# Optimization experiments

Measured on AMD Instinct MI355X. Metric: run time of the kernel, lower is better.

The kernel has to match this reference:

```python
import jax, jax.numpy as jnp
import numpy as np

NUM_MOL = 1024
KE = 14.399645351950548
KEHALF = KE / 2.0
CUTOFF = 10.0  # PhysNetCutOff(10.0)


def physnet_cutoff(d):
    # PhysNet smooth cutoff: 1 - 6u^5 + 15u^4 - 10u^3 for d < rc, else 0
    u = d / CUTOFF
    fc = 1.0 - 6.0 * u**5 + 15.0 * u**4 - 10.0 * u**3
    return jnp.where(d < CUTOFF, fc, 0.0)


def setup_inputs() -> dict:
    key = jax.random.key(0)
    k = jax.random.split(key, 5)
    N, E = 100000, 3200000
    # atomic numbers as floats in [1, 94]
    Z = jax.random.randint(k[0], (N,), 1, 95).astype(jnp.float32)
    # pair displacement vectors; norm ~ O(3) Angstrom, well inside cutoff
    r_ij = jax.random.normal(k[1], (E, 3), dtype=jnp.float32) * 2.0
    idx_i = jax.random.randint(k[2], (E,), 0, N, dtype=jnp.int32)
    idx_j = jax.random.randint(k[3], (E,), 0, N, dtype=jnp.int32)
    # per-atom molecule index, sorted (maxm = idx_m[-1] + 1 in the original)
    idx_m = jnp.sort(jax.random.randint(k[4], (N,), 0, NUM_MOL, dtype=jnp.int32))
    adiv = jnp.ones((1,), jnp.float32)
    apow = jnp.ones((1,), jnp.float32)
    a_vector = jnp.ones((4,), jnp.float32)
    c_vector = jnp.ones((4,), jnp.float32)
    return dict(Z=Z, r_ij=r_ij, idx_i=idx_i, idx_j=idx_j, idx_m=idx_m,
                adiv=adiv, apow=apow, a_vector=a_vector, c_vector=c_vector)


def reference(Z, r_ij, idx_i, idx_j, idx_m, adiv, apow, a_vector, c_vector):
    N = Z.shape[0]
    d = jnp.linalg.norm(r_ij, axis=1)                      # (E,)
    cut = physnet_cutoff(d)                                # (E,)
    z = Z ** jax.nn.softplus(apow[0])                      # (N,)
    a = (z[idx_i] + z[idx_j]) * jax.nn.softplus(adiv[0])   # (E,)
    a_comp = jax.nn.softplus(a_vector)[:, None] * a        # (4, E)
    c = jax.nn.softplus(c_vector)
    c_normed = c / jnp.sum(jnp.abs(c))                     # L1-normalize over dim 0
    f_temp = jnp.einsum('k,ke->e', c_normed, jnp.exp(-a_comp * d))  # (E,)
    f = f_temp * cut
    zizj = Z[idx_i] * Z[idx_j]
    e_edge = KEHALF * f * zizj / d                          # (E,)
    y_atom = jax.ops.segment_sum(e_edge, idx_i, num_segments=N)        # (N,)
    y = jax.ops.segment_sum(y_atom, idx_m, num_segments=NUM_MOL)       # (NUM_MOL,)
    return y
```

## Files before the change

### kernel.cpp

```cpp
#include <hip/hip_runtime.h>

#define NUM_MOL 1024
#define KEHALF 7.199822675975274f
#define RCUT 10.0f
#define ZS_CAP 130048

__device__ __forceinline__ float softplus_f(float x) {
    return (x > 20.0f) ? x : __logf(1.0f + __expf(x));
}

__device__ __forceinline__ float uni(float x) {
    return __int_as_float(__builtin_amdgcn_readfirstlane(__float_as_int(x)));
}


struct SmemT {
    float zptab[256];
    unsigned char zs[ZS_CAP];
};

__global__ __launch_bounds__(1024, 4) void zbl_edge_lds(
    const float4* __restrict__ r4,
    const int4* __restrict__ idx_i4,
    const int4* __restrict__ idx_j4,
    const int* __restrict__ idx_i,
    const int* __restrict__ idx_j,
    const float* __restrict__ r_ij,
    const float* __restrict__ Z,
    const int* __restrict__ idx_m,
    const float* __restrict__ adiv,
    const float* __restrict__ apow,
    const float* __restrict__ a_vector,
    const float* __restrict__ c_vector,
    float* __restrict__ y, int N, int E)
{
    __shared__ SmemT sm;
    const int tid = threadIdx.x;

    {
        const int nv4 = N >> 2;
        const float4* Z4 = (const float4*)Z;
        uchar4* dst = (uchar4*)sm.zs;
        for (int k = tid; k < nv4; k += blockDim.x) {
            const float4 zv = Z4[k];
            uchar4 pk;
            pk.x = (unsigned char)(int)zv.x;
            pk.y = (unsigned char)(int)zv.y;
            pk.z = (unsigned char)(int)zv.z;
            pk.w = (unsigned char)(int)zv.w;
            dst[k] = pk;
        }
        for (int k = (nv4 << 2) + tid; k < N; k += blockDim.x)
            sm.zs[k] = (unsigned char)(int)Z[k];
        if (tid < 256) {
            const float p = softplus_f(apow[0]);
            sm.zptab[tid] = (tid > 0) ? __powf((float)tid, p) : 0.0f;
        }
    }

    const float sp_adiv = uni(softplus_f(adiv[0]));
    const float sa0 = uni(softplus_f(a_vector[0]));
    const float sa1 = uni(softplus_f(a_vector[1]));
    const float sa2 = uni(softplus_f(a_vector[2]));
    const float sa3 = uni(softplus_f(a_vector[3]));
    float c0 = softplus_f(c_vector[0]);
    float c1 = softplus_f(c_vector[1]);
    float c2 = softplus_f(c_vector[2]);
    float c3 = softplus_f(c_vector[3]);
    const float cinv = 1.0f / (fabsf(c0) + fabsf(c1) + fabsf(c2) + fabsf(c3));
    const float k0 = uni(c0 * cinv);
    const float k1 = uni(c1 * cinv);
    const float k2 = uni(c2 * cinv);
    const float k3 = uni(c3 * cinv);
    const float samin = uni(fminf(fminf(sa0, sa1), fminf(sa2, sa3)));

    __syncthreads();

    auto edge1 = [&](int i, int j, float d2) {
        const int zi = sm.zs[i];
        const int zj = sm.zs[j];
        const float zpi = sm.zptab[zi];
        const float zpj = sm.zptab[zj];
        const float rinv = rsqrtf(d2);
        const float d = d2 * rinv;
        const float ad = (zpi + zpj) * sp_adiv * d;
        if (ad * samin < 104.0f) {
            const float u = d * (1.0f / RCUT);
            const float u3 = u * u * u;
            float fc = 1.0f + u3 * (-10.0f + u * (15.0f - 6.0f * u));
            fc = (d < RCUT) ? fc : 0.0f;
            const float ft = k0 * __expf(-sa0 * ad) + k1 * __expf(-sa1 * ad)
                           + k2 * __expf(-sa2 * ad) + k3 * __expf(-sa3 * ad);
            const float ee = KEHALF * ft * fc * (float)(zi * zj) * rinv;
            if (ee != 0.0f) atomicAdd(&y[idx_m[i]], ee);
        }
    };
    auto edge4 = [&](const int4& vi, const int4& vj,
                     const float4& r0, const float4& r1, const float4& r2) {
        edge1(vi.x, vj.x, r0.x * r0.x + r0.y * r0.y + r0.z * r0.z);
        edge1(vi.y, vj.y, r0.w * r0.w + r1.x * r1.x + r1.y * r1.y);
        edge1(vi.z, vj.z, r1.z * r1.z + r1.w * r1.w + r2.x * r2.x);
        edge1(vi.w, vj.w, r2.y * r2.y + r2.z * r2.z + r2.w * r2.w);
    };

    const int t = blockIdx.x * blockDim.x + tid;
    const int nthr = gridDim.x * blockDim.x;
    const int E4 = E >> 2;

#define LOADG(s, g) \
    int4 vi##s, vj##s; float4 ra##s, rb##s, rc##s; \
    const bool act##s = (g) < E4; \
    if (act##s) { vi##s = idx_i4[(g)]; vj##s = idx_j4[(g)]; \
        ra##s = r4[3 * (g) + 0]; rb##s = r4[3 * (g) + 1]; rc##s = r4[3 * (g) + 2]; }
#define COMPG(s) if (act##s) edge4(vi##s, vj##s, ra##s, rb##s, rc##s);

    for (int gb = t; gb < E4; gb += 4 * nthr) {
        const int g0 = gb;
        const int g1 = gb + nthr;
        const int g2 = gb + 2 * nthr;
        const int g3 = gb + 3 * nthr;
        LOADG(0, g0) LOADG(1, g1) LOADG(2, g2) LOADG(3, g3)
        COMPG(0) COMPG(1) COMPG(2) COMPG(3)
    }
#undef LOADG
#undef COMPG

    for (int e = (E4 << 2) + t; e < E; e += nthr) {
        const float x  = r_ij[3 * e + 0];
        const float yy = r_ij[3 * e + 1];
        const float zz = r_ij[3 * e + 2];
        edge1(idx_i[e], idx_j[e], x * x + yy * yy + zz * zz);
    }
}

__global__ __launch_bounds__(256) void zbl_edge_kernel_nows(
    const float* __restrict__ r_ij,
    const int* __restrict__ idx_i,
    const int* __restrict__ idx_j,
    const float* __restrict__ Z,
    const int* __restrict__ idx_m,
    const float* __restrict__ adiv,
    const float* __restrict__ apow,
    const float* __restrict__ a_vector,
    const float* __restrict__ c_vector,
    float* __restrict__ y, int E)
{
    __shared__ float bins[NUM_MOL];
    for (int b = threadIdx.x; b < NUM_MOL; b += blockDim.x) bins[b] = 0.0f;
    __syncthreads();

    const float sp_apow = softplus_f(apow[0]);
    const float sp_adiv = softplus_f(adiv[0]);
    const float sa0 = softplus_f(a_vector[0]);
    const float sa1 = softplus_f(a_vector[1]);
    const float sa2 = softplus_f(a_vector[2]);
    const float sa3 = softplus_f(a_vector[3]);
    float c0 = softplus_f(c_vector[0]);
    float c1 = softplus_f(c_vector[1]);
    float c2 = softplus_f(c_vector[2]);
    float c3 = softplus_f(c_vector[3]);
    const float cs = fabsf(c0) + fabsf(c1) + fabsf(c2) + fabsf(c3);
    const float cinv = 1.0f / cs;
    c0 *= cinv; c1 *= cinv; c2 *= cinv; c3 *= cinv;

    const int stride = gridDim.x * blockDim.x;
    for (int e = blockIdx.x * blockDim.x + threadIdx.x; e < E; e += stride) {
        const int i = idx_i[e];
        const int j = idx_j[e];
        const float zi = Z[i];
        const float zj = Z[j];
        const float x  = r_ij[3 * e + 0];
        const float yy = r_ij[3 * e + 1];
        const float zz = r_ij[3 * e + 2];
        const float d = sqrtf(x * x + yy * yy + zz * zz);

        const float u = d * (1.0f / RCUT);
        const float u3 = u * u * u;
        float fc = 1.0f + u3 * (-10.0f + u * (15.0f - 6.0f * u));
        fc = (d < RCUT) ? fc : 0.0f;

        const float a = (__powf(zi, sp_apow) + __powf(zj, sp_apow)) * sp_adiv;
        const float ad = a * d;
        const float ft = c0 * __expf(-sa0 * ad) + c1 * __expf(-sa1 * ad)
                       + c2 * __expf(-sa2 * ad) + c3 * __expf(-sa3 * ad);

        const float ee = KEHALF * ft * fc * zi * zj / d;
        if (ee != 0.0f) atomicAdd(&bins[idx_m[i]], ee);
    }

    __syncthreads();
    for (int b = threadIdx.x; b < NUM_MOL; b += blockDim.x) {
        const float v = bins[b];
        if (v != 0.0f) atomicAdd(&y[b], v);
    }
}

extern "C" void kernel_launch(void* const* d_in, const int* in_sizes, int n_in,
                              void* d_out, int out_size, void* d_ws, size_t ws_size,
                              hipStream_t stream) {
    const float* Z        = (const float*)d_in[0];
    const float* r_ij     = (const float*)d_in[1];
    const int*   idx_i    = (const int*)d_in[2];
    const int*   idx_j    = (const int*)d_in[3];
    const int*   idx_m    = (const int*)d_in[4];
    const float* adiv     = (const float*)d_in[5];
    const float* apow     = (const float*)d_in[6];
    const float* a_vector = (const float*)d_in[7];
    const float* c_vector = (const float*)d_in[8];
    float* y = (float*)d_out;

    const int N = in_sizes[0];
    const int E = in_sizes[1] / 3;

    hipMemsetAsync(y, 0, (size_t)out_size * sizeof(float), stream);

    if (N <= ZS_CAP) {
        zbl_edge_lds<<<256, 1024, 0, stream>>>(
            (const float4*)r_ij, (const int4*)idx_i, (const int4*)idx_j,
            idx_i, idx_j, r_ij, Z, idx_m, adiv, apow, a_vector, c_vector,
            y, N, E);
    } else {
        zbl_edge_kernel_nows<<<2048, 256, 0, stream>>>(r_ij, idx_i, idx_j, Z, idx_m,
                                                       adiv, apow, a_vector, c_vector, y, E);
    }
}
```

Before: 128.7 us.

## Move per-atom Z byte table from per-block LDS to a global L2-resident workspace

Adds a small prep kernel that packs Z into a uint8 array and builds a pow-table pre-scaled by softplus(adiv) in the workspace. The edge kernel then gathers Z bytes from global memory (L2) instead of having every one of the 256 blocks copy the whole 100K-entry array into about 130KB of LDS. This removes the large per-block staging cost and the LDS-driven single-block occupancy, and launches 2048 blocks of 256 threads. It also computes sqrt only and defers rsqrt until the exponential threshold passes, and drops the 4-way load batching. The trade-off is random global gathers through L2 in place of LDS reads, plus one extra kernel launch.

```diff
diff --git a/kernel.cpp b/kernel.cpp
--- a/kernel.cpp
+++ b/kernel.cpp
@@ -3,7 +3,6 @@
 #define NUM_MOL 1024
 #define KEHALF 7.199822675975274f
 #define RCUT 10.0f
-#define ZS_CAP 130048
 
 __device__ __forceinline__ float softplus_f(float x) {
     return (x > 20.0f) ? x : __logf(1.0f + __expf(x));
@@ -13,52 +12,51 @@
     return __int_as_float(__builtin_amdgcn_readfirstlane(__float_as_int(x)));
 }
 
-
-struct SmemT {
-    float zptab[256];
-    unsigned char zs[ZS_CAP];
-};
-
-__global__ __launch_bounds__(1024, 4) void zbl_edge_lds(
+__global__ __launch_bounds__(256) void zbl_prep(
+    const float* __restrict__ Z,
+    const float* __restrict__ apow,
+    const float* __restrict__ adiv,
+    float* __restrict__ zptab_g,
+    unsigned char* __restrict__ zu8, int N)
+{
+    const int n4 = blockIdx.x * blockDim.x + threadIdx.x;
+    const int nv4 = N >> 2;
+    if (n4 < nv4) {
+        const float4 zv = ((const float4*)Z)[n4];
+        uchar4 pk;
+        pk.x = (unsigned char)(int)zv.x;
+        pk.y = (unsigned char)(int)zv.y;
+        pk.z = (unsigned char)(int)zv.z;
+        pk.w = (unsigned char)(int)zv.w;
+        ((uchar4*)zu8)[n4] = pk;
+    }
+    const int base = nv4 << 2;
+    if (n4 < N - base) zu8[base + n4] = (unsigned char)(int)Z[base + n4];
+    if (blockIdx.x == 0 && threadIdx.x < 256) {
+        const float p = softplus_f(apow[0]);
+        const float s = softplus_f(adiv[0]);
+        const int t = threadIdx.x;
+        zptab_g[t] = (t > 0) ? __powf((float)t, p) * s : 0.0f;
+    }
+}
+
+__global__ __launch_bounds__(256, 8) void zbl_edge_l2(
     const float4* __restrict__ r4,
     const int4* __restrict__ idx_i4,
     const int4* __restrict__ idx_j4,
     const int* __restrict__ idx_i,
     const int* __restrict__ idx_j,
     const float* __restrict__ r_ij,
-    const float* __restrict__ Z,
+    const unsigned char* __restrict__ zu8,
+    const float* __restrict__ zptab_g,
     const int* __restrict__ idx_m,
-    const float* __restrict__ adiv,
-    const float* __restrict__ apow,
     const float* __restrict__ a_vector,
     const float* __restrict__ c_vector,
-    float* __restrict__ y, int N, int E)
+    float* __restrict__ y, int E)
 {
-    __shared__ SmemT sm;
-    const int tid = threadIdx.x;
-
-    {
-        const int nv4 = N >> 2;
-        const float4* Z4 = (const float4*)Z;
-        uchar4* dst = (uchar4*)sm.zs;
-        for (int k = tid; k < nv4; k += blockDim.x) {
-            const float4 zv = Z4[k];
-            uchar4 pk;
-            pk.x = (unsigned char)(int)zv.x;
-            pk.y = (unsigned char)(int)zv.y;
-            pk.z = (unsigned char)(int)zv.z;
-            pk.w = (unsigned char)(int)zv.w;
-            dst[k] = pk;
-        }
-        for (int k = (nv4 << 2) + tid; k < N; k += blockDim.x)
-            sm.zs[k] = (unsigned char)(int)Z[k];
-        if (tid < 256) {
-            const float p = softplus_f(apow[0]);
-            sm.zptab[tid] = (tid > 0) ? __powf((float)tid, p) : 0.0f;
-        }
-    }
-
-    const float sp_adiv = uni(softplus_f(adiv[0]));
+    __shared__ float zptab[256];
+    zptab[threadIdx.x] = zptab_g[threadIdx.x];
+
     const float sa0 = uni(softplus_f(a_vector[0]));
     const float sa1 = uni(softplus_f(a_vector[1]));
     const float sa2 = uni(softplus_f(a_vector[2]));
@@ -72,19 +70,20 @@
     const float k1 = uni(c1 * cinv);
     const float k2 = uni(c2 * cinv);
     const float k3 = uni(c3 * cinv);
-    const float samin = uni(fminf(fminf(sa0, sa1), fminf(sa2, sa3)));
+    const float samin = fminf(fminf(sa0, sa1), fminf(sa2, sa3));
+    const float C2 = uni(104.0f / samin);
 
     __syncthreads();
 
     auto edge1 = [&](int i, int j, float d2) {
-        const int zi = sm.zs[i];
-        const int zj = sm.zs[j];
-        const float zpi = sm.zptab[zi];
-        const float zpj = sm.zptab[zj];
-        const float rinv = rsqrtf(d2);
-        const float d = d2 * rinv;
-        const float ad = (zpi + zpj) * sp_adiv * d;
-        if (ad * samin < 104.0f) {
+        const int zi = zu8[i];
+        const int zj = zu8[j];
+        const float si = zptab[zi];
+        const float sj = zptab[zj];
+        const float d = sqrtf(d2);
+        const float ad = (si + sj) * d;
+        if (ad < C2) {
+            const float rinv = rsqrtf(d2);
             const float u = d * (1.0f / RCUT);
             const float u3 = u * u * u;
             float fc = 1.0f + u3 * (-10.0f + u * (15.0f - 6.0f * u));
@@ -95,35 +94,22 @@
             if (ee != 0.0f) atomicAdd(&y[idx_m[i]], ee);
         }
     };
-    auto edge4 = [&](const int4& vi, const int4& vj,
-                     const float4& r0, const float4& r1, const float4& r2) {
+
+    const int t = blockIdx.x * blockDim.x + threadIdx.x;
+    const int nthr = gridDim.x * blockDim.x;
+    const int E4 = E >> 2;
+
+    for (int g = t; g < E4; g += nthr) {
+        const int4 vi = idx_i4[g];
+        const int4 vj = idx_j4[g];
+        const float4 r0 = r4[3 * g + 0];
+        const float4 r1 = r4[3 * g + 1];
+        const float4 r2 = r4[3 * g + 2];
         edge1(vi.x, vj.x, r0.x * r0.x + r0.y * r0.y + r0.z * r0.z);
         edge1(vi.y, vj.y, r0.w * r0.w + r1.x * r1.x + r1.y * r1.y);
         edge1(vi.z, vj.z, r1.z * r1.z + r1.w * r1.w + r2.x * r2.x);
         edge1(vi.w, vj.w, r2.y * r2.y + r2.z * r2.z + r2.w * r2.w);
-    };
-
-    const int t = blockIdx.x * blockDim.x + tid;
-    const int nthr = gridDim.x * blockDim.x;
-    const int E4 = E >> 2;
-
-#define LOADG(s, g) \
-    int4 vi##s, vj##s; float4 ra##s, rb##s, rc##s; \
-    const bool act##s = (g) < E4; \
-    if (act##s) { vi##s = idx_i4[(g)]; vj##s = idx_j4[(g)]; \
-        ra##s = r4[3 * (g) + 0]; rb##s = r4[3 * (g) + 1]; rc##s = r4[3 * (g) + 2]; }
-#define COMPG(s) if (act##s) edge4(vi##s, vj##s, ra##s, rb##s, rc##s);
-
-    for (int gb = t; gb < E4; gb += 4 * nthr) {
-        const int g0 = gb;
-        const int g1 = gb + nthr;
-        const int g2 = gb + 2 * nthr;
-        const int g3 = gb + 3 * nthr;
-        LOADG(0, g0) LOADG(1, g1) LOADG(2, g2) LOADG(3, g3)
-        COMPG(0) COMPG(1) COMPG(2) COMPG(3)
-    }
-#undef LOADG
-#undef COMPG
+    }
 
     for (int e = (E4 << 2) + t; e < E; e += nthr) {
         const float x  = r_ij[3 * e + 0];
@@ -214,11 +200,16 @@
 
     hipMemsetAsync(y, 0, (size_t)out_size * sizeof(float), stream);
 
-    if (N <= ZS_CAP) {
-        zbl_edge_lds<<<256, 1024, 0, stream>>>(
+    const size_t ws_need = 1024 + (size_t)N + 16;
+    if (ws_size >= ws_need) {
+        float* zptab_g = (float*)d_ws;
+        unsigned char* zu8 = (unsigned char*)d_ws + 1024;
+        zbl_prep<<<(N / 4 + 255) / 256 + 1, 256, 0, stream>>>(
+            Z, apow, adiv, zptab_g, zu8, N);
+        zbl_edge_l2<<<2048, 256, 0, stream>>>(
             (const float4*)r_ij, (const int4*)idx_i, (const int4*)idx_j,
-            idx_i, idx_j, r_ij, Z, idx_m, adiv, apow, a_vector, c_vector,
-            y, N, E);
+            idx_i, idx_j, r_ij, zu8, zptab_g, idx_m,
+            a_vector, c_vector, y, E);
     } else {
         zbl_edge_kernel_nows<<<2048, 256, 0, stream>>>(r_ij, idx_i, idx_j, Z, idx_m,
                                                        adiv, apow, a_vector, c_vector, y, E);
```

Measured after the change: 133.8 us. +4.0%, slower.
